# Kernel tuning notes

Hardware: AMD Instinct MI355X
Metric: run time of the kernel (lower is better)

## Reference

```python
import jax, jax.numpy as jnp
import numpy as np

N = 100000        # nodes
E = 3200000       # directed edges (before self-loops)
IN_CH = 500
HID = 256
HEADS = 8
C = HID // HEADS  # 32 per-head channels
OUT_CH = 40
NEG_SLOPE = 0.2   # PyG GATConv default


def _gat_conv(x, W, a_src, a_dst, b, src, dst):
    """PyG-style GATConv (concat=True, self-loops already in src/dst, eval mode)."""
    n = x.shape[0]
    h = (x @ W).reshape(n, HEADS, C)                      # [N, H, C]
    # per-node attention logits
    e_src = jnp.einsum('nhc,hc->nh', h, a_src)            # source contribution
    e_dst = jnp.einsum('nhc,hc->nh', h, a_dst)            # target contribution
    e = jax.nn.leaky_relu(e_src[src] + e_dst[dst], NEG_SLOPE)  # [E, H]
    # segment softmax over incoming edges of each destination node
    m = jax.ops.segment_max(e, dst, num_segments=n)       # [N, H]
    e = jnp.exp(e - m[dst])
    s = jax.ops.segment_sum(e, dst, num_segments=n)       # [N, H]
    alpha = e / (s[dst] + 1e-16)                          # [E, H]
    msg = h[src] * alpha[:, :, None]                      # [E, H, C]
    out = jax.ops.segment_sum(msg, dst, num_segments=n)   # [N, H, C]
    return out.reshape(n, HEADS * C) + b


def setup_inputs() -> dict:
    key = jax.random.key(0)
    ks = jax.random.split(key, 20)
    x = jax.random.normal(ks[0], (N, IN_CH), jnp.float32)
    edge_index = jax.random.randint(ks[1], (2, E), 0, N, dtype=jnp.int64)

    def glorot(k, shape):
        fan = shape[0] + shape[-1]
        return jax.random.normal(k, shape, jnp.float32) * jnp.sqrt(2.0 / fan)

    inp = {"x": x, "edge_index": edge_index}
    in_dims = [IN_CH, HID, HID]
    for i in range(3):
        inp[f"W{i}"] = glorot(ks[2 + 4 * i], (in_dims[i], HID))
        inp[f"a_src{i}"] = glorot(ks[3 + 4 * i], (HEADS, C))
        inp[f"a_dst{i}"] = glorot(ks[4 + 4 * i], (HEADS, C))
        inp[f"b{i}"] = jnp.zeros((HID,), jnp.float32)
    inp["Wf"] = glorot(ks[15], (HID, OUT_CH))
    inp["bf"] = jnp.zeros((OUT_CH,), jnp.float32)
    return inp


def reference(x, edge_index, W0, a_src0, a_dst0, b0, W1, a_src1, a_dst1, b1,
              W2, a_src2, a_dst2, b2, Wf, bf):
    # add self loops (PyG GATConv default)
    loop = jnp.arange(N, dtype=edge_index.dtype)
    src = jnp.concatenate([edge_index[0], loop])
    dst = jnp.concatenate([edge_index[1], loop])

    h0 = jax.nn.elu(_gat_conv(x, W0, a_src0, a_dst0, b0, src, dst))
    h1 = jax.nn.elu(_gat_conv(h0, W1, a_src1, a_dst1, b1, src, dst))
    h2 = _gat_conv(h1, W2, a_src2, a_dst2, b2, src, dst)  # last conv: no activation
    # JumpingKnowledge 'max': elementwise max over layer outputs
    jk = jnp.maximum(jnp.maximum(h0, h1), h2)
    logits = jk @ Wf + bf
    return jax.nn.log_softmax(logits, axis=1)
```

## Files before the change

kernel.cpp:

```cpp
#include <hip/hip_runtime.h>
#include <hip/hip_bf16.h>
#include <math.h>

#define HID 256
#define HEADS 8
#define KP0 512
#define EPB 16384
#define NBMAX 1024

typedef __attribute__((ext_vector_type(8))) short short8;
typedef __attribute__((ext_vector_type(4))) float floatx4;

__device__ __forceinline__ void gl_lds16(const void* g, void* l) {
  __builtin_amdgcn_global_load_lds(
      (const __attribute__((address_space(1))) void*)g,
      (__attribute__((address_space(3))) void*)l, 16, 0, 0);
}


__global__ __launch_bounds__(256) void edge_hist_kernel(const int* __restrict__ ei,
    int* __restrict__ F, int E, int Etot, int NB, int NBLK) {
  __shared__ int hist[NBMAX];
  int blk = blockIdx.x, t = threadIdx.x;
  for (int i = t; i < NBMAX; i += 256) hist[i] = 0;
  __syncthreads();
  int base = blk * EPB;
  int lim = min(EPB, Etot - base);
  for (int i = t; i < lim; i += 256) {
    int idx = base + i;
    int d = (idx < E) ? ei[E + idx] : (idx - E);
    atomicAdd(&hist[d >> 7], 1);
  }
  __syncthreads();
  for (int b = t; b < NB; b += 256) F[b * NBLK + blk] = hist[b];
}


__global__ __launch_bounds__(256) void scan_part_kernel(const int* __restrict__ F,
    int* __restrict__ bsum, int L) {
  __shared__ int ws[4];
  int blk = blockIdx.x, t = threadIdx.x;
  int base = blk * 1024 + t * 4;
  int s = 0;
  if (base + 3 < L) {
    int4 v = *(const int4*)(F + base);
    s = v.x + v.y + v.z + v.w;
  } else {
    for (int i = 0; i < 4; ++i) if (base + i < L) s += F[base + i];
  }
#pragma unroll
  for (int off = 1; off < 64; off <<= 1) s += __shfl_xor(s, off);
  if ((t & 63) == 0) ws[t >> 6] = s;
  __syncthreads();
  if (t == 0) bsum[blk] = ws[0] + ws[1] + ws[2] + ws[3];
}

__global__ __launch_bounds__(256) void scan_bsum_kernel(const int* __restrict__ bsum,
    int* __restrict__ bb, int* __restrict__ S, int NBS, int L) {
  __shared__ int ps[256];
  int t = threadIdx.x;
  int v = (t < NBS) ? bsum[t] : 0;
  ps[t] = v;
  __syncthreads();
  for (int off = 1; off < 256; off <<= 1) {
    int add = (t >= off) ? ps[t - off] : 0;
    __syncthreads();
    ps[t] += add;
    __syncthreads();
  }
  if (t < NBS) bb[t] = (t == 0) ? 0 : ps[t - 1];
  if (t == 255) S[L] = ps[255];
}

__global__ __launch_bounds__(256) void scan_apply_kernel(const int* __restrict__ F,
    const int* __restrict__ bb, int* __restrict__ S, int L) {
  __shared__ int ps[256];
  int blk = blockIdx.x, t = threadIdx.x;
  int base = blk * 1024 + t * 4;
  int v0 = 0, v1 = 0, v2 = 0, v3 = 0;
  if (base + 3 < L) {
    int4 w = *(const int4*)(F + base);
    v0 = w.x; v1 = w.y; v2 = w.z; v3 = w.w;
  } else {
    if (base + 0 < L) v0 = F[base + 0];
    if (base + 1 < L) v1 = F[base + 1];
    if (base + 2 < L) v2 = F[base + 2];
    if (base + 3 < L) v3 = F[base + 3];
  }
  ps[t] = v0 + v1 + v2 + v3;
  __syncthreads();
  for (int off = 1; off < 256; off <<= 1) {
    int add = (t >= off) ? ps[t - off] : 0;
    __syncthreads();
    ps[t] += add;
    __syncthreads();
  }
  int run = bb[blk] + ((t == 0) ? 0 : ps[t - 1]);
  if (base + 0 < L) S[base + 0] = run; run += v0;
  if (base + 1 < L) S[base + 1] = run; run += v1;
  if (base + 2 < L) S[base + 2] = run; run += v2;
  if (base + 3 < L) S[base + 3] = run;
}

__global__ __launch_bounds__(256) void edge_scatter_kernel(const int* __restrict__ ei,
    const int* __restrict__ S, unsigned* __restrict__ stag, int E, int Etot,
    int NB, int NBLK) {
  __shared__ int cur[NBMAX];
  int blk = blockIdx.x, t = threadIdx.x;
  for (int b = t; b < NB; b += 256) cur[b] = S[b * NBLK + blk];
  __syncthreads();
  int base = blk * EPB;
  int lim = min(EPB, Etot - base);
  for (int i = t; i < lim; i += 256) {
    int idx = base + i;
    int s, d;
    if (idx < E) { s = ei[idx]; d = ei[E + idx]; }
    else { s = idx - E; d = s; }
    int pos = atomicAdd(&cur[d >> 7], 1);
    stag[pos] = ((unsigned)(d & 127) << 17) | (unsigned)s;
  }
}

__global__ __launch_bounds__(256) void bucket_build_kernel(const unsigned* __restrict__ stag,
    const int* __restrict__ S, int NBLK,
    int* __restrict__ rowptr, int* __restrict__ csr_src, int N) {
  __shared__ int deg[128], pfx[128], cur[128];
  int b = blockIdx.x;
  int t = threadIdx.x;
  int gbase = S[(size_t)b * NBLK];
  int gend = S[(size_t)(b + 1) * NBLK];
  int cnt = gend - gbase;
  int node0 = b << 7;
  int nn = min(128, N - node0);
  if (t < 128) deg[t] = 0;
  __syncthreads();
  const unsigned* sb = stag + gbase;
  for (int i = t; i < cnt; i += 256) atomicAdd(&deg[sb[i] >> 17], 1);
  __syncthreads();
  if (t == 0) {
    int run = 0;
#pragma unroll 8
    for (int i = 0; i < 128; ++i) { pfx[i] = run; run += deg[i]; }
  }
  __syncthreads();
  if (t < 128) cur[t] = pfx[t];
  if (t < nn) rowptr[node0 + t] = gbase + pfx[t];
  if (b == (int)gridDim.x - 1 && t == 0) rowptr[N] = gbase + cnt;
  __syncthreads();
  for (int i = t; i < cnt; i += 256) {
    unsigned v = sb[i];
    int dl = v >> 17;
    int pos = gbase + atomicAdd(&cur[dl], 1);
    csr_src[pos] = (int)(v & 0x1ffff);
  }
}


__global__ __launch_bounds__(256) void conv_x_kernel(const float* __restrict__ x,
    __hip_bfloat16* __restrict__ xb, int M, int K) {
  long idx = (long)blockIdx.x * 256 + threadIdx.x;
  if (idx >= (long)M * (KP0 / 8)) return;
  int n = (int)(idx >> 6);
  int k0 = ((int)idx & 63) * 8;
  const float* xr = x + (size_t)n * K;
  float4 a = {0.f, 0.f, 0.f, 0.f}, b = {0.f, 0.f, 0.f, 0.f};
  if (k0 + 3 < K) a = *(const float4*)(xr + k0);
  else {
    if (k0 + 0 < K) a.x = xr[k0 + 0];
    if (k0 + 1 < K) a.y = xr[k0 + 1];
    if (k0 + 2 < K) a.z = xr[k0 + 2];
    if (k0 + 3 < K) a.w = xr[k0 + 3];
  }
  if (k0 + 7 < K) b = *(const float4*)(xr + k0 + 4);
  else {
    if (k0 + 4 < K) b.x = xr[k0 + 4];
    if (k0 + 5 < K) b.y = xr[k0 + 5];
    if (k0 + 6 < K) b.z = xr[k0 + 6];
    if (k0 + 7 < K) b.w = xr[k0 + 7];
  }
  union { short8 v; __hip_bfloat16 h[8]; } o;
  o.h[0] = __float2bfloat16(a.x); o.h[1] = __float2bfloat16(a.y);
  o.h[2] = __float2bfloat16(a.z); o.h[3] = __float2bfloat16(a.w);
  o.h[4] = __float2bfloat16(b.x); o.h[5] = __float2bfloat16(b.y);
  o.h[6] = __float2bfloat16(b.z); o.h[7] = __float2bfloat16(b.w);
  *(short8*)(xb + (size_t)n * KP0 + k0) = o.v;
}

__global__ __launch_bounds__(256) void convT_w_kernel(const float* __restrict__ W,
    __hip_bfloat16* __restrict__ Wt, int K, int Kp) {
  int idx = blockIdx.x * 256 + threadIdx.x;
  if (idx >= 256 * Kp) return;
  int n = idx / Kp, k = idx - n * Kp;
  Wt[idx] = __float2bfloat16((k < K) ? W[(size_t)k * 256 + n] : 0.f);
}


__global__ __launch_bounds__(256) void gemm_mfma(const __hip_bfloat16* __restrict__ A,
    const __hip_bfloat16* __restrict__ Bt, __hip_bfloat16* __restrict__ C,
    int M, int Kp) {
  __shared__ __align__(16) __hip_bfloat16 As[128][32];
  __shared__ __align__(16) __hip_bfloat16 Bs[128][32];
  int tid = threadIdx.x;
  int wave = tid >> 6, lane = tid & 63;
  int quad = lane >> 4, mr = lane & 15;
  int row0 = blockIdx.x * 128, col0 = blockIdx.y * 128;
  int wm = (wave & 1) * 64, wn = (wave >> 1) * 64;
  floatx4 acc[4][4] = {};

  int srow = (lane >> 2);
  int kslot = lane & 3;
  int kc = (kslot ^ (srow & 3)) * 8;

  for (int k0 = 0; k0 < Kp; k0 += 32) {
#pragma unroll
    for (int j = 0; j < 2; ++j) {
      int r = wave * 32 + j * 16 + srow;
      gl_lds16(A + (size_t)(row0 + r) * Kp + k0 + kc, &As[wave * 32 + j * 16][0]);
      gl_lds16(Bt + (size_t)(col0 + r) * Kp + k0 + kc, &Bs[wave * 32 + j * 16][0]);
    }
    __syncthreads();
    short8 af[4], bfr[4];
#pragma unroll
    for (int r = 0; r < 4; ++r) {
      int row = wm + r * 16 + mr;
      af[r] = *(const short8*)&As[row][(quad ^ (row & 3)) * 8];
      int col = wn + r * 16 + mr;
      bfr[r] = *(const short8*)&Bs[col][(quad ^ (col & 3)) * 8];
    }
#pragma unroll
    for (int r = 0; r < 4; ++r)
#pragma unroll
      for (int c = 0; c < 4; ++c)
        acc[r][c] = __builtin_amdgcn_mfma_f32_16x16x32_bf16(af[r], bfr[c], acc[r][c], 0, 0, 0);
    __syncthreads();
  }
#pragma unroll
  for (int r = 0; r < 4; ++r) {
#pragma unroll
    for (int c = 0; c < 4; ++c) {
#pragma unroll
      for (int i = 0; i < 4; ++i) {
        int row = row0 + wm + r * 16 + quad * 4 + i;
        int col = col0 + wn + c * 16 + mr;
        if (row < M) C[(size_t)row * HID + col] = __float2bfloat16(acc[r][c][i]);
      }
    }
  }
}


__global__ __launch_bounds__(256) void node_logits_kernel(const __hip_bfloat16* __restrict__ H,
    const float* __restrict__ a_src, const float* __restrict__ a_dst,
    float* __restrict__ en_src, float* __restrict__ en_dst, int N) {
  int idx = blockIdx.x * 256 + threadIdx.x;
  if (idx >= N * HEADS) return;
  int n = idx >> 3, h = idx & 7;
  const uint4* Hp = (const uint4*)(H + (size_t)n * HID + h * 32);
  const float* S = a_src + h * 32;
  const float* D = a_dst + h * 32;
  float es = 0.f, ed = 0.f;
#pragma unroll
  for (int j = 0; j < 4; ++j) {
    uint4 u = Hp[j];
    unsigned w[4] = {u.x, u.y, u.z, u.w};
#pragma unroll
    for (int p = 0; p < 4; ++p) {
      float lo = __uint_as_float(w[p] << 16);
      float hi = __uint_as_float(w[p] & 0xffff0000u);
      int c = j * 8 + p * 2;
      es += lo * S[c] + hi * S[c + 1];
      ed += lo * D[c] + hi * D[c + 1];
    }
  }
  en_src[idx] = es;
  en_dst[idx] = ed;
}


__global__ __launch_bounds__(256) void gat_agg_kernel(const __hip_bfloat16* __restrict__ H,
    const float* __restrict__ en_src, const float* __restrict__ en_dst,
    const int* __restrict__ rowptr, const int* __restrict__ csr_src,
    const float* __restrict__ bias, float* __restrict__ out,
    __hip_bfloat16* __restrict__ hb, int apply_elu, int N) {
  int wave = threadIdx.x >> 6;
  int lane = threadIdx.x & 63;
  int n = blockIdx.x * 4 + wave;
  if (n >= N) return;
  int h = lane >> 3;
  int slot = lane & 7;
  int beg = rowptr[n], end = rowptr[n + 1];
  float ed = en_dst[n * HEADS + h];

  float m = -1e30f, s = 0.f;
  for (int e = beg + slot; e < end; e += 8) {
    int src = csr_src[e];
    float v = en_src[src * HEADS + h] + ed;
    v = (v > 0.f) ? v : 0.2f * v;
    float mn = fmaxf(m, v);
    s = s * __expf(m - mn) + __expf(v - mn);
    m = mn;
  }
#pragma unroll
  for (int off = 1; off < 8; off <<= 1) {
    float mo = __shfl_xor(m, off);
    float so = __shfl_xor(s, off);
    float mn = fmaxf(m, mo);
    s = s * __expf(m - mn) + so * __expf(mo - mn);
    m = mn;
  }
  float rs = 1.f / (s + 1e-16f);

  float4 acc = {0.f, 0.f, 0.f, 0.f};
  const __hip_bfloat16* Hc = H + lane * 4;
  for (int cs = beg; cs < end; cs += 64) {
    int cnt = min(64, end - cs);
    int myidx = csr_src[cs + ((lane < cnt) ? lane : (cnt - 1))];
    int i = 0;
    for (; i + 4 <= cnt; i += 4) {
      int s0 = __shfl(myidx, i);
      int s1 = __shfl(myidx, i + 1);
      int s2 = __shfl(myidx, i + 2);
      int s3 = __shfl(myidx, i + 3);
      uint2 g0 = *(const uint2*)(Hc + (size_t)s0 * HID);
      uint2 g1 = *(const uint2*)(Hc + (size_t)s1 * HID);
      uint2 g2 = *(const uint2*)(Hc + (size_t)s2 * HID);
      uint2 g3 = *(const uint2*)(Hc + (size_t)s3 * HID);
      float e0 = en_src[s0 * HEADS + h];
      float e1 = en_src[s1 * HEADS + h];
      float e2 = en_src[s2 * HEADS + h];
      float e3 = en_src[s3 * HEADS + h];
      uint2 gs[4] = {g0, g1, g2, g3};
      float es4[4] = {e0, e1, e2, e3};
#pragma unroll
      for (int j = 0; j < 4; ++j) {
        float v = es4[j] + ed;
        v = (v > 0.f) ? v : 0.2f * v;
        float w = __expf(v - m) * rs;
        uint2 g = gs[j];
        acc.x += w * __uint_as_float(g.x << 16);
        acc.y += w * __uint_as_float(g.x & 0xffff0000u);
        acc.z += w * __uint_as_float(g.y << 16);
        acc.w += w * __uint_as_float(g.y & 0xffff0000u);
      }
    }
    for (; i < cnt; ++i) {
      int s0 = __shfl(myidx, i);
      uint2 g = *(const uint2*)(Hc + (size_t)s0 * HID);
      float v = en_src[s0 * HEADS + h] + ed;
      v = (v > 0.f) ? v : 0.2f * v;
      float w = __expf(v - m) * rs;
      acc.x += w * __uint_as_float(g.x << 16);
      acc.y += w * __uint_as_float(g.x & 0xffff0000u);
      acc.z += w * __uint_as_float(g.y << 16);
      acc.w += w * __uint_as_float(g.y & 0xffff0000u);
    }
  }
  float4 bv = *(const float4*)(bias + lane * 4);
  float4 o;
  o.x = acc.x + bv.x; o.y = acc.y + bv.y; o.z = acc.z + bv.z; o.w = acc.w + bv.w;
  if (apply_elu) {
    o.x = (o.x > 0.f) ? o.x : expm1f(o.x);
    o.y = (o.y > 0.f) ? o.y : expm1f(o.y);
    o.z = (o.z > 0.f) ? o.z : expm1f(o.z);
    o.w = (o.w > 0.f) ? o.w : expm1f(o.w);
  }
  *(float4*)(out + (size_t)n * HID + lane * 4) = o;
  union { __hip_bfloat16 hh[4]; uint2 u; } pk;
  pk.hh[0] = __float2bfloat16(o.x);
  pk.hh[1] = __float2bfloat16(o.y);
  pk.hh[2] = __float2bfloat16(o.z);
  pk.hh[3] = __float2bfloat16(o.w);
  *(uint2*)(hb + (size_t)n * HID + lane * 4) = pk.u;
}


__global__ __launch_bounds__(256) void final_kernel(const float* __restrict__ h0,
    const float* __restrict__ h1, const float* __restrict__ h2,
    const float* __restrict__ Wf, const float* __restrict__ bf,
    float* __restrict__ out, int N) {
  __shared__ float Wfs[HID * 40];
  __shared__ float jks[4][HID];
  int tid = threadIdx.x;
  for (int i = tid; i < HID * 40; i += 256) Wfs[i] = Wf[i];
  int sub = tid >> 6, lane = tid & 63;
  int n = blockIdx.x * 4 + sub;
  if (n < N) {
    const float4* p0 = (const float4*)(h0 + (size_t)n * HID);
    const float4* p1 = (const float4*)(h1 + (size_t)n * HID);
    const float4* p2 = (const float4*)(h2 + (size_t)n * HID);
    float4 a = p0[lane], b = p1[lane], cc = p2[lane];
    float4 r;
    r.x = fmaxf(fmaxf(a.x, b.x), cc.x);
    r.y = fmaxf(fmaxf(a.y, b.y), cc.y);
    r.z = fmaxf(fmaxf(a.z, b.z), cc.z);
    r.w = fmaxf(fmaxf(a.w, b.w), cc.w);
    *(float4*)&jks[sub][lane * 4] = r;
  }
  __syncthreads();
  float logit = -INFINITY;
  if (lane < 40 && n < N) {
    float accv = bf[lane];
#pragma unroll 8
    for (int k = 0; k < HID; ++k) accv += jks[sub][k] * Wfs[k * 40 + lane];
    logit = accv;
  }
  float mx = logit;
#pragma unroll
  for (int off = 32; off > 0; off >>= 1) mx = fmaxf(mx, __shfl_down(mx, off));
  mx = __shfl(mx, 0);
  float ex = (lane < 40 && n < N) ? __expf(logit - mx) : 0.f;
  float sm = ex;
#pragma unroll
  for (int off = 32; off > 0; off >>= 1) sm += __shfl_down(sm, off);
  sm = __shfl(sm, 0);
  if (lane < 40 && n < N) out[(size_t)n * 40 + lane] = logit - mx - __logf(sm);
}


extern "C" void kernel_launch(void* const* d_in, const int* in_sizes, int n_in,
                              void* d_out, int out_size, void* d_ws, size_t ws_size,
                              hipStream_t stream) {
  (void)n_in; (void)out_size; (void)ws_size;
  const float* x   = (const float*)d_in[0];
  const int*   ei  = (const int*)d_in[1];
  const float* W0  = (const float*)d_in[2];
  const float* as0 = (const float*)d_in[3];
  const float* ad0 = (const float*)d_in[4];
  const float* b0  = (const float*)d_in[5];
  const float* W1  = (const float*)d_in[6];
  const float* as1 = (const float*)d_in[7];
  const float* ad1 = (const float*)d_in[8];
  const float* b1  = (const float*)d_in[9];
  const float* W2  = (const float*)d_in[10];
  const float* as2 = (const float*)d_in[11];
  const float* ad2 = (const float*)d_in[12];
  const float* b2  = (const float*)d_in[13];
  const float* Wf  = (const float*)d_in[14];
  const float* bf  = (const float*)d_in[15];
  float* out = (float*)d_out;

  const int E = in_sizes[1] / 2;
  const int IN_CH = in_sizes[2] / HID;
  const int N = in_sizes[0] / IN_CH;
  const int Etot = E + N;
  const int Mp = ((N + 127) / 128) * 128;
  const int NB = (N + 127) >> 7;
  const int NBLK = (Etot + EPB - 1) / EPB;
  const int L = NB * NBLK;
  const int NBS = (L + 1023) / 1024;
  const size_t NM = (size_t)N * HID;

  __hip_bfloat16* xb  = (__hip_bfloat16*)d_ws;
  __hip_bfloat16* Htb = xb + (size_t)Mp * KP0;
  __hip_bfloat16* hb  = Htb + NM;
  __hip_bfloat16* Wt0 = hb + (size_t)Mp * HID;
  __hip_bfloat16* Wt1 = Wt0 + 256 * KP0;
  __hip_bfloat16* Wt2 = Wt1 + 256 * 256;
  float* fbase = (float*)(Wt2 + 256 * 256);
  float* h0   = fbase;
  float* h1   = fbase + NM;
  float* h2   = fbase + 2 * NM;
  float* en_s = fbase + 3 * NM;
  float* en_d = en_s + (size_t)N * HEADS;
  int* rowptr  = (int*)(en_d + (size_t)N * HEADS);
  int* csr_src = rowptr + (((size_t)N + 1 + 3) & ~(size_t)3);
  int* F       = csr_src + (((size_t)Etot + 3) & ~(size_t)3);
  int* S       = F + (((size_t)L + 3) & ~(size_t)3);
  int* bsum    = S + (((size_t)L + 1 + 3) & ~(size_t)3);
  int* bb      = bsum + 256;
  unsigned* stag = (unsigned*)(bb + 256);

  edge_hist_kernel<<<NBLK, 256, 0, stream>>>(ei, F, E, Etot, NB, NBLK);
  scan_part_kernel<<<NBS, 256, 0, stream>>>(F, bsum, L);
  scan_bsum_kernel<<<1, 256, 0, stream>>>(bsum, bb, S, NBS, L);
  scan_apply_kernel<<<NBS, 256, 0, stream>>>(F, bb, S, L);
  edge_scatter_kernel<<<NBLK, 256, 0, stream>>>(ei, S, stag, E, Etot, NB, NBLK);
  bucket_build_kernel<<<NB, 256, 0, stream>>>(stag, S, NBLK, rowptr, csr_src, N);

  conv_x_kernel<<<((size_t)N * (KP0 / 8) + 255) / 256, 256, 0, stream>>>(x, xb, N, IN_CH);
  convT_w_kernel<<<(256 * KP0 + 255) / 256, 256, 0, stream>>>(W0, Wt0, IN_CH, KP0);
  convT_w_kernel<<<(256 * 256 + 255) / 256, 256, 0, stream>>>(W1, Wt1, HID, HID);
  convT_w_kernel<<<(256 * 256 + 255) / 256, 256, 0, stream>>>(W2, Wt2, HID, HID);

  dim3 ggrid(Mp / 128, 2);
  int lblocks = (N * HEADS + 255) / 256;
  int ablocks = (N + 3) / 4;

  gemm_mfma<<<ggrid, 256, 0, stream>>>(xb, Wt0, Htb, N, KP0);
  node_logits_kernel<<<lblocks, 256, 0, stream>>>(Htb, as0, ad0, en_s, en_d, N);
  gat_agg_kernel<<<ablocks, 256, 0, stream>>>(Htb, en_s, en_d, rowptr, csr_src, b0, h0, hb, 1, N);
  gemm_mfma<<<ggrid, 256, 0, stream>>>(hb, Wt1, Htb, N, HID);
  node_logits_kernel<<<lblocks, 256, 0, stream>>>(Htb, as1, ad1, en_s, en_d, N);
  gat_agg_kernel<<<ablocks, 256, 0, stream>>>(Htb, en_s, en_d, rowptr, csr_src, b1, h1, hb, 1, N);
  gemm_mfma<<<ggrid, 256, 0, stream>>>(hb, Wt2, Htb, N, HID);
  node_logits_kernel<<<lblocks, 256, 0, stream>>>(Htb, as2, ad2, en_s, en_d, N);
  gat_agg_kernel<<<ablocks, 256, 0, stream>>>(Htb, en_s, en_d, rowptr, csr_src, b2, h2, hb, 0, N);

  final_kernel<<<(N + 3) / 4, 256, 0, stream>>>(h0, h1, h2, Wf, bf, out, N);
}
```

Baseline: 1.772 ms.

## Split wave into two half-waves each gathering 16-byte rows of alternate edges

The aggregation kernel now has each half of the 64-lane wave handle alternate edges. Each lane loads 8 bf16 values (16 bytes) per source row instead of 4, and the two halves' partial sums are combined with a cross-half shuffle at the end. Softmax stats (max, reciprocal sum, dst logit) are redistributed by shuffle to match the new head mapping, and outputs are written with nontemporal stores. The aim is fewer, wider gather instructions and more edges in flight per wave. The cost is an extra reduction and half the lanes sitting idle during the epilogue.

```diff
diff --git a/kernel.cpp b/kernel.cpp
--- a/kernel.cpp
+++ b/kernel.cpp
@@ -10,11 +10,22 @@
 
 typedef __attribute__((ext_vector_type(8))) short short8;
 typedef __attribute__((ext_vector_type(4))) float floatx4;
+typedef __attribute__((ext_vector_type(4))) unsigned uintx4;
 
 __device__ __forceinline__ void gl_lds16(const void* g, void* l) {
   __builtin_amdgcn_global_load_lds(
       (const __attribute__((address_space(1))) void*)g,
       (__attribute__((address_space(3))) void*)l, 16, 0, 0);
+}
+
+__device__ __forceinline__ float blo(unsigned u) { return __uint_as_float(u << 16); }
+__device__ __forceinline__ float bhi(unsigned u) { return __uint_as_float(u & 0xffff0000u); }
+
+__device__ __forceinline__ void acc8(float* acc, uintx4 g, float w) {
+  acc[0] += w * blo(g[0]); acc[1] += w * bhi(g[0]);
+  acc[2] += w * blo(g[1]); acc[3] += w * bhi(g[1]);
+  acc[4] += w * blo(g[2]); acc[5] += w * bhi(g[2]);
+  acc[6] += w * blo(g[3]); acc[7] += w * bhi(g[3]);
 }
 
 
@@ -34,7 +45,6 @@
   __syncthreads();
   for (int b = t; b < NB; b += 256) F[b * NBLK + blk] = hist[b];
 }
-
 
 __global__ __launch_bounds__(256) void scan_part_kernel(const int* __restrict__ F,
     int* __restrict__ bsum, int L) {
@@ -241,7 +251,7 @@
 #pragma unroll
       for (int i = 0; i < 4; ++i) {
         int row = row0 + wm + r * 16 + quad * 4 + i;
-        int col = col0 + wn + c * 16 + mr;
+        int col = wn + c * 16 + mr + col0;
         if (row < M) C[(size_t)row * HID + col] = __float2bfloat16(acc[r][c][i]);
       }
     }
@@ -265,8 +275,8 @@
     unsigned w[4] = {u.x, u.y, u.z, u.w};
 #pragma unroll
     for (int p = 0; p < 4; ++p) {
-      float lo = __uint_as_float(w[p] << 16);
-      float hi = __uint_as_float(w[p] & 0xffff0000u);
+      float lo = blo(w[p]);
+      float hi = bhi(w[p]);
       int c = j * 8 + p * 2;
       es += lo * S[c] + hi * S[c + 1];
       ed += lo * D[c] + hi * D[c + 1];
@@ -310,67 +320,69 @@
   }
   float rs = 1.f / (s + 1e-16f);
 
-  float4 acc = {0.f, 0.f, 0.f, 0.f};
-  const __hip_bfloat16* Hc = H + lane * 4;
+  int eo = lane >> 5;
+  int cl = lane & 31;
+  int hh = cl >> 2;
+  float m2 = __shfl(m, hh * 8);
+  float rs2 = __shfl(rs, hh * 8);
+  float ed2 = __shfl(ed, hh * 8);
+
+  float acc[8] = {0.f, 0.f, 0.f, 0.f, 0.f, 0.f, 0.f, 0.f};
+  const __hip_bfloat16* Hc = H + cl * 8;
   for (int cs = beg; cs < end; cs += 64) {
     int cnt = min(64, end - cs);
     int myidx = csr_src[cs + ((lane < cnt) ? lane : (cnt - 1))];
     int i = 0;
     for (; i + 4 <= cnt; i += 4) {
-      int s0 = __shfl(myidx, i);
-      int s1 = __shfl(myidx, i + 1);
-      int s2 = __shfl(myidx, i + 2);
-      int s3 = __shfl(myidx, i + 3);
-      uint2 g0 = *(const uint2*)(Hc + (size_t)s0 * HID);
-      uint2 g1 = *(const uint2*)(Hc + (size_t)s1 * HID);
-      uint2 g2 = *(const uint2*)(Hc + (size_t)s2 * HID);
-      uint2 g3 = *(const uint2*)(Hc + (size_t)s3 * HID);
-      float e0 = en_src[s0 * HEADS + h];
-      float e1 = en_src[s1 * HEADS + h];
-      float e2 = en_src[s2 * HEADS + h];
-      float e3 = en_src[s3 * HEADS + h];
-      uint2 gs[4] = {g0, g1, g2, g3};
-      float es4[4] = {e0, e1, e2, e3};
-#pragma unroll
-      for (int j = 0; j < 4; ++j) {
-        float v = es4[j] + ed;
-        v = (v > 0.f) ? v : 0.2f * v;
-        float w = __expf(v - m) * rs;
-        uint2 g = gs[j];
-        acc.x += w * __uint_as_float(g.x << 16);
-        acc.y += w * __uint_as_float(g.x & 0xffff0000u);
-        acc.z += w * __uint_as_float(g.y << 16);
-        acc.w += w * __uint_as_float(g.y & 0xffff0000u);
-      }
-    }
-    for (; i < cnt; ++i) {
-      int s0 = __shfl(myidx, i);
-      uint2 g = *(const uint2*)(Hc + (size_t)s0 * HID);
-      float v = en_src[s0 * HEADS + h] + ed;
-      v = (v > 0.f) ? v : 0.2f * v;
-      float w = __expf(v - m) * rs;
-      acc.x += w * __uint_as_float(g.x << 16);
-      acc.y += w * __uint_as_float(g.x & 0xffff0000u);
-      acc.z += w * __uint_as_float(g.y << 16);
-      acc.w += w * __uint_as_float(g.y & 0xffff0000u);
-    }
-  }
-  float4 bv = *(const float4*)(bias + lane * 4);
-  float4 o;
-  o.x = acc.x + bv.x; o.y = acc.y + bv.y; o.z = acc.z + bv.z; o.w = acc.w + bv.w;
-  if (apply_elu) {
-    o.x = (o.x > 0.f) ? o.x : expm1f(o.x);
-    o.y = (o.y > 0.f) ? o.y : expm1f(o.y);
-    o.z = (o.z > 0.f) ? o.z : expm1f(o.z);
-    o.w = (o.w > 0.f) ? o.w : expm1f(o.w);
-  }
-  *(float4*)(out + (size_t)n * HID + lane * 4) = o;
-  union { __hip_bfloat16 hh[4]; uint2 u; } pk;
-  pk.hh[0] = __float2bfloat16(o.x);
-  pk.hh[1] = __float2bfloat16(o.y);
-  pk.hh[2] = __float2bfloat16(o.z);
-  pk.hh[3] = __float2bfloat16(o.w);
-  *(uint2*)(hb + (size_t)n * HID + lane * 4) = pk.u;
+      int sa = __shfl(myidx, i + eo);
+      int sb = __shfl(myidx, i + 2 + eo);
+      uintx4 ga = *(const uintx4*)(Hc + (size_t)sa * HID);
+      uintx4 gb = *(const uintx4*)(Hc + (size_t)sb * HID);
+      float va = en_src[sa * HEADS + hh] + ed2;
+      float vb = en_src[sb * HEADS + hh] + ed2;
+      va = (va > 0.f) ? va : 0.2f * va;
+      vb = (vb > 0.f) ? vb : 0.2f * vb;
+      float wa = __expf(va - m2) * rs2;
+      float wb = __expf(vb - m2) * rs2;
+      acc8(acc, ga, wa);
+      acc8(acc, gb, wb);
+    }
+    for (; i < cnt; i += 2) {
+      int j = i + eo;
+      int jj = (j < cnt) ? j : (cnt - 1);
+      int sa = __shfl(myidx, jj);
+      uintx4 ga = *(const uintx4*)(Hc + (size_t)sa * HID);
+      float va = en_src[sa * HEADS + hh] + ed2;
+      va = (va > 0.f) ? va : 0.2f * va;
+      float wa = (j < cnt) ? __expf(va - m2) * rs2 : 0.f;
+      acc8(acc, ga, wa);
+    }
+  }
+#pragma unroll
+  for (int i = 0; i < 8; ++i) acc[i] += __shfl_xor(acc[i], 32);
+
+  if (eo == 0) {
+    const float4* bp = (const float4*)(bias + cl * 8);
+    float4 b0 = bp[0], b1 = bp[1];
+    float o[8];
+    o[0] = acc[0] + b0.x; o[1] = acc[1] + b0.y;
+    o[2] = acc[2] + b0.z; o[3] = acc[3] + b0.w;
+    o[4] = acc[4] + b1.x; o[5] = acc[5] + b1.y;
+    o[6] = acc[6] + b1.z; o[7] = acc[7] + b1.w;
+    if (apply_elu) {
+#pragma unroll
+      for (int i = 0; i < 8; ++i) o[i] = (o[i] > 0.f) ? o[i] : expm1f(o[i]);
+    }
+    floatx4 f0 = {o[0], o[1], o[2], o[3]};
+    floatx4 f1 = {o[4], o[5], o[6], o[7]};
+    float* op = out + (size_t)n * HID + cl * 8;
+    __builtin_nontemporal_store(f0, (floatx4*)op);
+    __builtin_nontemporal_store(f1, (floatx4*)(op + 4));
+    union { __hip_bfloat16 hh8[8]; uintx4 u; } pk;
+#pragma unroll
+    for (int i = 0; i < 8; ++i) pk.hh8[i] = __float2bfloat16(o[i]);
+    __builtin_nontemporal_store(pk.u, (uintx4*)(hb + (size_t)n * HID + cl * 8));
+  }
 }
 
 
```

Result: no change. 1.785 ms (+0.7%).
